# Optimization experiments

Hardware: AMD Instinct MI355X
Metric: run time of the kernel (lower is better)

Reference implementation:

```python
import jax, jax.numpy as jnp
import numpy as np

B, N, C = 4, 2048, 2048
H = 16
D = C // H  # head dim = 128


def setup_inputs() -> dict:
    key = jax.random.key(0)
    ks = jax.random.split(key, 5)
    s = 1.0 / np.sqrt(C)
    x = jax.random.normal(ks[0], (B, N, C), dtype=jnp.float32)
    w_qkv = jax.random.normal(ks[1], (C, 3 * C), dtype=jnp.float32) * s
    b_qkv = jax.random.normal(ks[2], (3 * C,), dtype=jnp.float32) * 0.01
    w_proj = jax.random.normal(ks[3], (C, C), dtype=jnp.float32) * s
    b_proj = jax.random.normal(ks[4], (C,), dtype=jnp.float32) * 0.01
    return {"x": x, "w_qkv": w_qkv, "b_qkv": b_qkv, "w_proj": w_proj, "b_proj": b_proj}


def reference(x, w_qkv, b_qkv, w_proj, b_proj):
    scale = D ** (-0.5)
    qkv = x @ w_qkv + b_qkv                              # [B,N,3C]
    qkv = qkv.reshape(B, N, 3, H, D).transpose(2, 0, 3, 1, 4)  # [3,B,H,N,D]
    q, k, v = qkv[0], qkv[1], qkv[2]
    attn = jnp.einsum('bhnd,bhmd->bhnm', q, k) * scale   # [B,H,N,N]
    attn = jax.nn.softmax(attn, axis=-1)
    out = jnp.einsum('bhnm,bhmd->bhnd', attn, v)         # [B,H,N,D]
    out = out.transpose(0, 2, 1, 3).reshape(B, N, C)
    return out @ w_proj + b_proj
```

## Files before the change

### kernel.cpp

```cpp
#include <hip/hip_runtime.h>

typedef short bf16x8 __attribute__((ext_vector_type(8)));
typedef float f32x4 __attribute__((ext_vector_type(4)));
typedef float f32x16 __attribute__((ext_vector_type(16)));
typedef unsigned int u32x4 __attribute__((ext_vector_type(4)));
typedef unsigned short u16;
typedef unsigned int u32;

__device__ __forceinline__ u16 f2bf(float f) {
  unsigned u = __builtin_bit_cast(unsigned, f);
  u += 0x7fffu + ((u >> 16) & 1u);
  return (u16)(u >> 16);
}

__device__ __forceinline__ void async16(const void* g, void* l) {
  __builtin_amdgcn_global_load_lds(
      (const __attribute__((address_space(1))) void*)g,
      (__attribute__((address_space(3))) void*)l, 16, 0, 0);
}

__global__ __launch_bounds__(256) void k_cvt(const float* __restrict__ src,
                                             u16* __restrict__ dst, int n4) {
  int i = blockIdx.x * blockDim.x + threadIdx.x;
  int stride = gridDim.x * blockDim.x;
  for (; i < n4; i += stride) {
    float4 f = ((const float4*)src)[i];
    ushort4 o;
    o.x = f2bf(f.x); o.y = f2bf(f.y); o.z = f2bf(f.z); o.w = f2bf(f.w);
    ((ushort4*)dst)[i] = o;
  }
}

__global__ __launch_bounds__(256) void k_tcvt(const float* __restrict__ src,
                                              u16* __restrict__ dst,
                                              int R, int C) {
  __shared__ float tile[64][65];
  int c0 = blockIdx.x * 64, r0 = blockIdx.y * 64;
  int tx = threadIdx.x & 63, ty = threadIdx.x >> 6;
#pragma unroll
  for (int i = 0; i < 64; i += 4)
    tile[ty + i][tx] = src[(size_t)(r0 + ty + i) * C + c0 + tx];
  __syncthreads();
#pragma unroll
  for (int i = 0; i < 64; i += 4)
    dst[(size_t)(c0 + ty + i) * R + r0 + tx] = f2bf(tile[tx][ty + i]);
}


__device__ __forceinline__ void stage_tile(u16* lds, const u16* gsrc, int tid) {
  const int r0 = tid >> 3, sl = tid & 7;
#pragma unroll
  for (int h = 0; h < 2; h++)
#pragma unroll
    for (int cc = 0; cc < 2; cc++) {
      int row = r0 + cc * 64;
      async16(gsrc + (size_t)(h * 128 + row) * 2048 + ((sl ^ (row & 7)) << 3),
              (char*)lds + ((size_t)(h * 1024 + row * 8 + sl) << 4));
    }
}

template <int QM>
__device__ __forceinline__ void rd_a(bf16x8 (&dst)[4][2], const u16* base,
                                     int lo, int g) {
#pragma unroll
  for (int m2 = 0; m2 < 4; m2++)
#pragma unroll
    for (int ks = 0; ks < 2; ks++) {
      int row = QM * 64 + m2 * 16 + lo;
      dst[m2][ks] = *(const bf16x8*)((const char*)base + row * 128 +
                                     (((ks * 4 + g) ^ (row & 7)) << 4));
    }
}

template <int QN>
__device__ __forceinline__ void rd_b(bf16x8 (&dst)[2][2], const u16* base,
                                     int brow_base, int lo, int g) {
#pragma unroll
  for (int n2 = 0; n2 < 2; n2++)
#pragma unroll
    for (int ks = 0; ks < 2; ks++) {
      int row = brow_base + QN * 32 + n2 * 16 + lo;
      dst[n2][ks] = *(const bf16x8*)((const char*)base + row * 128 +
                                     (((ks * 4 + g) ^ (row & 7)) << 4));
    }
}

template <int QM, int QN>
__device__ __forceinline__ void do_mm(f32x4 (&acc)[8][4], bf16x8 (&fa)[4][2],
                                      bf16x8 (&fb)[2][2]) {
  __builtin_amdgcn_s_setprio(1);
#pragma unroll
  for (int m2 = 0; m2 < 4; m2++)
#pragma unroll
    for (int n2 = 0; n2 < 2; n2++)
#pragma unroll
      for (int ks = 0; ks < 2; ks++)
        acc[QM * 4 + m2][QN * 2 + n2] = __builtin_amdgcn_mfma_f32_16x16x32_bf16(
            fa[m2][ks], fb[n2][ks], acc[QM * 4 + m2][QN * 2 + n2], 0, 0, 0);
  __builtin_amdgcn_s_setprio(0);
}

template <int EPI, int NT>
__global__ __launch_bounds__(512, 2) void k_gemm(
    const u16* __restrict__ A, const u16* __restrict__ Bt,
    const float* __restrict__ bias,
    u16* __restrict__ qb, u16* __restrict__ kb, u16* __restrict__ vtb,
    float* __restrict__ fout) {
  __shared__ u16 aL[2][2][128 * 64];
  __shared__ u16 bL[2][2][128 * 64];
  const int tid = threadIdx.x;
  const int lane = tid & 63, w = tid >> 6;
  const int lo = lane & 15, g = lane >> 4;
  const int wm = w >> 2, wn = w & 3;
  const int brow_base = (wn & 1) * 64;
  const int nwg = NT * 32;
  const int swz = (blockIdx.x & 7) * (nwg >> 3) + (blockIdx.x >> 3);
  const int by = swz / NT, bx = swz % NT;
  const int rm0 = by * 256, cn0 = bx * 256;
  const u16* Ab = A + (size_t)rm0 * 2048;
  const u16* Bb = Bt + (size_t)cn0 * 2048;

  f32x4 acc[8][4];
#pragma unroll
  for (int i = 0; i < 8; i++)
#pragma unroll
    for (int j = 0; j < 4; j++) {
      acc[i][j][0] = 0.f; acc[i][j][1] = 0.f;
      acc[i][j][2] = 0.f; acc[i][j][3] = 0.f;
    }

  stage_tile(&aL[0][0][0], Ab, tid);
  stage_tile(&bL[0][0][0], Bb, tid);

  for (int it = 0; it < 16; ++it) {
#pragma unroll
    for (int tt = 0; tt < 2; ++tt) {
      const int tn = 2 * it + tt + 1;
      const u16* aS = &aL[tt][wm][0];
      const u16* bS = &bL[tt][wn >> 1][0];
      bf16x8 fa[4][2], fb0[2][2], fb1[2][2];
      if (tn < 32) {
        stage_tile(&aL[tt ^ 1][0][0], Ab + tn * 64, tid);
        stage_tile(&bL[tt ^ 1][0][0], Bb + tn * 64, tid);
        asm volatile("s_waitcnt vmcnt(8)" ::: "memory");
      } else {
        asm volatile("s_waitcnt vmcnt(0)" ::: "memory");
      }
      __builtin_amdgcn_s_barrier();
      rd_a<0>(fa, aS, lo, g);
      rd_b<0>(fb0, bS, brow_base, lo, g);
      asm volatile("s_waitcnt lgkmcnt(0)" ::: "memory");
      do_mm<0, 0>(acc, fa, fb0);
      rd_b<1>(fb1, bS, brow_base, lo, g);
      asm volatile("s_waitcnt lgkmcnt(0)" ::: "memory");
      do_mm<0, 1>(acc, fa, fb1);
      rd_a<1>(fa, aS, lo, g);
      asm volatile("s_waitcnt lgkmcnt(0)" ::: "memory");
      do_mm<1, 1>(acc, fa, fb1);
      do_mm<1, 0>(acc, fa, fb0);
      __builtin_amdgcn_s_barrier();
    }
  }

#pragma unroll
  for (int qi = 0; qi < 8; qi++) {
    const int rowb = rm0 + wm * 128 + (qi >> 2) * 64 + (qi & 3) * 16 + g * 4;
#pragma unroll
    for (int nj = 0; nj < 4; nj++) {
      const int col = cn0 + wn * 64 + (nj >> 1) * 32 + (nj & 1) * 16 + lo;
      const float bcol = bias[col];
      const float v0 = acc[qi][nj][0] + bcol, v1 = acc[qi][nj][1] + bcol;
      const float v2 = acc[qi][nj][2] + bcol, v3 = acc[qi][nj][3] + bcol;
      if constexpr (EPI == 0) {
        const int which = col >> 11;
        const int hc = col & 2047, d = hc & 127;
        const int bh = ((rowb >> 11) << 4) | (hc >> 7);
        if (which == 2) {
          ushort4 us;
          us.x = f2bf(v0); us.y = f2bf(v1); us.z = f2bf(v2); us.w = f2bf(v3);
          *(ushort4*)(vtb + (size_t)bh * 262144 + (size_t)d * 2048 +
                      (rowb & 2047)) = us;
        } else {
          u16* dst = (which == 0) ? qb : kb;
          const float sc = (which == 0) ? 0.12751743f : 1.0f;
          size_t base = (size_t)bh * 262144 + (size_t)(rowb & 2047) * 128 + d;
          dst[base] = f2bf(v0 * sc);
          dst[base + 128] = f2bf(v1 * sc);
          dst[base + 256] = f2bf(v2 * sc);
          dst[base + 384] = f2bf(v3 * sc);
        }
      } else {
        fout[(size_t)(rowb + 0) * 2048 + col] = v0;
        fout[(size_t)(rowb + 1) * 2048 + col] = v1;
        fout[(size_t)(rowb + 2) * 2048 + col] = v2;
        fout[(size_t)(rowb + 3) * 2048 + col] = v3;
      }
    }
  }
}

__global__ __launch_bounds__(512) void k_attn(
    const u16* __restrict__ qg, const u16* __restrict__ kg,
    const u16* __restrict__ vtg, u16* __restrict__ og) {
  __shared__ u16 kt[2][64 * 128];
  __shared__ u16 vt[2][128 * 64];
  const int bh = blockIdx.x;
  const int b = bh >> 4, h = bh & 15;
  const u16* Q = qg + (size_t)bh * 262144;
  const u16* Kp = kg + (size_t)bh * 262144;
  const u16* VT = vtg + (size_t)bh * 262144;
  const int tid = threadIdx.x;
  const int lane = tid & 63, w = tid >> 6;
  const int ql = lane & 31, hi = lane >> 5;
  const int q0 = blockIdx.y * 256 + w * 32;

  const int c0 = tid, c1 = tid + 512;
  const int kva = c0 >> 4, ksa = c0 & 15, kvb = c1 >> 4, ksb = c1 & 15;
  const size_t koff_a = (size_t)kva * 128 + (size_t)((ksa ^ (kva & 7)) * 8);
  const size_t koff_b = (size_t)kvb * 128 + (size_t)((ksb ^ (kvb & 7)) * 8);
  const int da = c0 >> 3, sva = c0 & 7, db = c1 >> 3, svb = c1 & 7;
  const size_t voff_a = (size_t)da * 2048 + (size_t)((sva ^ (da & 7)) * 8);
  const size_t voff_b = (size_t)db * 2048 + (size_t)((svb ^ (db & 7)) * 8);

  bf16x8 qf[8];
#pragma unroll
  for (int c = 0; c < 8; c++)
    qf[c] = *(const bf16x8*)(Q + (size_t)(q0 + ql) * 128 + c * 16 + hi * 8);

  f32x16 o[4];
#pragma unroll
  for (int nd = 0; nd < 4; nd++)
#pragma unroll
    for (int r = 0; r < 16; r++) o[nd][r] = 0.f;
  float m = -1e30f, l = 0.f;

  {
    async16(Kp + koff_a, &kt[0][c0 * 8]);
    async16(Kp + koff_b, &kt[0][c1 * 8]);
    async16(VT + voff_a, &vt[0][c0 * 8]);
    async16(VT + voff_b, &vt[0][c1 * 8]);
  }
  int cur = 0;
  for (int kv0 = 0; kv0 < 2048; kv0 += 64) {
    __syncthreads();
    if (kv0 + 64 < 2048) {
      const u16* kbp = Kp + (size_t)(kv0 + 64) * 128;
      const u16* vbp = VT + (kv0 + 64);
      int nx = cur ^ 1;
      async16(kbp + koff_a, &kt[nx][c0 * 8]);
      async16(kbp + koff_b, &kt[nx][c1 * 8]);
      async16(vbp + voff_a, &vt[nx][c0 * 8]);
      async16(vbp + voff_b, &vt[nx][c1 * 8]);
    }
    const char* ktb = (const char*)&kt[cur][0];
    const char* vtb = (const char*)&vt[cur][0];

    f32x16 sacc[2];
#pragma unroll
    for (int s2 = 0; s2 < 2; s2++)
#pragma unroll
      for (int r = 0; r < 16; r++) sacc[s2][r] = 0.f;
    __builtin_amdgcn_s_setprio(1);
#pragma unroll
    for (int c = 0; c < 8; c++)
#pragma unroll
      for (int s2 = 0; s2 < 2; s2++) {
        int kv = s2 * 32 + ql;
        int phys = kv * 256 + ((c * 32 + hi * 16) ^ ((kv & 7) << 4));
        bf16x8 kf = *(const bf16x8*)(ktb + phys);
        sacc[s2] = __builtin_amdgcn_mfma_f32_32x32x16_bf16(kf, qf[c], sacc[s2], 0, 0, 0);
      }
    __builtin_amdgcn_s_setprio(0);

    float tm = sacc[0][0];
#pragma unroll
    for (int r = 1; r < 16; r++) tm = fmaxf(tm, sacc[0][r]);
#pragma unroll
    for (int r = 0; r < 16; r++) tm = fmaxf(tm, sacc[1][r]);
    tm = fmaxf(tm, __shfl_xor(tm, 32));
    if (!__all(tm <= m)) {
      float mnew = fmaxf(m, tm);
      float corr = exp2f(m - mnew);
      l *= corr;
#pragma unroll
      for (int nd = 0; nd < 4; nd++)
#pragma unroll
        for (int r = 0; r < 16; r++) o[nd][r] *= corr;
      m = mnew;
    }
    float ps = 0.f;
#pragma unroll
    for (int s2 = 0; s2 < 2; s2++)
#pragma unroll
      for (int r = 0; r < 16; r++) {
        float p = exp2f(sacc[s2][r] - m);
        sacc[s2][r] = p;
        ps += p;
      }
    ps += __shfl_xor(ps, 32);
    l += ps;

    bf16x8 pf[4];
#pragma unroll
    for (int s2 = 0; s2 < 2; s2++) {
      u32 pk[8];
#pragma unroll
      for (int i = 0; i < 8; i++) {
        u32 t;
        asm("v_cvt_pk_bf16_f32 %0, %1, %2"
            : "=v"(t) : "v"(sacc[s2][2 * i]), "v"(sacc[s2][2 * i + 1]));
        pk[i] = t;
      }
#pragma unroll
      for (int ksl = 0; ksl < 2; ksl++) {
        u32 a0 = pk[4 * ksl + 0], b0 = pk[4 * ksl + 2];
        u32 a1 = pk[4 * ksl + 1], b1 = pk[4 * ksl + 3];
        asm("v_permlane32_swap_b32 %0, %1" : "+v"(a0), "+v"(b0));
        asm("v_permlane32_swap_b32 %0, %1" : "+v"(a1), "+v"(b1));
        u32x4 fr = {a0, a1, b0, b1};
        pf[s2 * 2 + ksl] = __builtin_bit_cast(bf16x8, fr);
      }
    }

    __builtin_amdgcn_s_setprio(1);
#pragma unroll
    for (int nd = 0; nd < 4; nd++)
#pragma unroll
      for (int ks = 0; ks < 4; ks++) {
        int d = nd * 32 + ql;
        int phys = d * 128 + ((ks * 32 + hi * 16) ^ ((d & 7) << 4));
        bf16x8 vf = *(const bf16x8*)(vtb + phys);
        o[nd] = __builtin_amdgcn_mfma_f32_32x32x16_bf16(vf, pf[ks], o[nd], 0, 0, 0);
      }
    __builtin_amdgcn_s_setprio(0);
    cur ^= 1;
  }

  float inv = 1.0f / l;
  size_t rowbase = ((size_t)(b * 2048 + q0 + ql)) * 2048 + h * 128 + hi * 4;
#pragma unroll
  for (int nd = 0; nd < 4; nd++)
#pragma unroll
    for (int j2 = 0; j2 < 4; j2++) {
      ushort4 us;
      us.x = f2bf(o[nd][4 * j2 + 0] * inv);
      us.y = f2bf(o[nd][4 * j2 + 1] * inv);
      us.z = f2bf(o[nd][4 * j2 + 2] * inv);
      us.w = f2bf(o[nd][4 * j2 + 3] * inv);
      *(ushort4*)(og + rowbase + nd * 32 + j2 * 8) = us;
    }
}

extern "C" void kernel_launch(void* const* d_in, const int* in_sizes, int n_in,
                              void* d_out, int out_size, void* d_ws, size_t ws_size,
                              hipStream_t stream) {
  const float* x      = (const float*)d_in[0];
  const float* w_qkv  = (const float*)d_in[1];
  const float* b_qkv  = (const float*)d_in[2];
  const float* w_proj = (const float*)d_in[3];
  const float* b_proj = (const float*)d_in[4];
  float* out = (float*)d_out;

  char* p = (char*)d_ws;
  u16* xb     = (u16*)p; p += (size_t)8192 * 2048 * 2;
  u16* wqkvT  = (u16*)p; p += (size_t)6144 * 2048 * 2;
  u16* wprojT = (u16*)p; p += (size_t)2048 * 2048 * 2;
  u16* qb     = (u16*)p; p += (size_t)64 * 2048 * 128 * 2;
  u16* kb     = (u16*)p; p += (size_t)64 * 2048 * 128 * 2;
  u16* vtb    = (u16*)p; p += (size_t)64 * 2048 * 128 * 2;

  k_cvt<<<2048, 256, 0, stream>>>(x, xb, (8192 * 2048) / 4);
  k_tcvt<<<dim3(6144 / 64, 2048 / 64), 256, 0, stream>>>(w_qkv, wqkvT, 2048, 6144);
  k_tcvt<<<dim3(2048 / 64, 2048 / 64), 256, 0, stream>>>(w_proj, wprojT, 2048, 2048);
  k_gemm<0, 24><<<768, 512, 0, stream>>>(xb, wqkvT, b_qkv, qb, kb, vtb, nullptr);
  k_attn<<<dim3(64, 8), 512, 0, stream>>>(qb, kb, vtb, xb);
  k_gemm<1, 8><<<256, 512, 0, stream>>>(xb, wprojT, b_proj, nullptr, nullptr, nullptr, out);
}
```

Baseline: 497.1 us.

## Process two 32-row query tiles per wave in attention, halving block threads

The attention kernel now launches 256 threads per block, and each wave handles 64 query rows as two 32-row tiles. Each K and V fragment read from LDS feeds two MFMAs, which halves LDS read traffic per FLOP and gives the scheduler more independent MFMA chains. Each thread now issues four async loads per buffer instead of two. The row-sum cross-lane reduction moves out of the loop into the epilogue. In exchange, register pressure roughly doubles (two sets of O accumulators and Q fragments), the launch bound is set to one block, and fewer waves are resident to hide latency.

New measurement: 562.5 us. +13.1%, slower.

```diff
diff --git a/kernel.cpp b/kernel.cpp
--- a/kernel.cpp
+++ b/kernel.cpp
@@ -199,7 +199,56 @@
   }
 }
 
-__global__ __launch_bounds__(512) void k_attn(
+__device__ __forceinline__ void softmax_pf(f32x16 (&sacc)[2], float& m,
+                                           float& l, f32x16 (&o)[4],
+                                           bf16x8 (&pf)[4]) {
+  float tm = sacc[0][0];
+#pragma unroll
+  for (int r = 1; r < 16; r++) tm = fmaxf(tm, sacc[0][r]);
+#pragma unroll
+  for (int r = 0; r < 16; r++) tm = fmaxf(tm, sacc[1][r]);
+  tm = fmaxf(tm, __shfl_xor(tm, 32));
+  if (!__all(tm <= m)) {
+    float mnew = fmaxf(m, tm);
+    float corr = exp2f(m - mnew);
+    l *= corr;
+#pragma unroll
+    for (int nd = 0; nd < 4; nd++)
+#pragma unroll
+      for (int r = 0; r < 16; r++) o[nd][r] *= corr;
+    m = mnew;
+  }
+#pragma unroll
+  for (int s2 = 0; s2 < 2; s2++)
+#pragma unroll
+    for (int r = 0; r < 16; r++) {
+      float p = exp2f(sacc[s2][r] - m);
+      sacc[s2][r] = p;
+      l += p;
+    }
+#pragma unroll
+  for (int s2 = 0; s2 < 2; s2++) {
+    u32 pk[8];
+#pragma unroll
+    for (int i = 0; i < 8; i++) {
+      u32 t;
+      asm("v_cvt_pk_bf16_f32 %0, %1, %2"
+          : "=v"(t) : "v"(sacc[s2][2 * i]), "v"(sacc[s2][2 * i + 1]));
+      pk[i] = t;
+    }
+#pragma unroll
+    for (int ksl = 0; ksl < 2; ksl++) {
+      u32 a0 = pk[4 * ksl + 0], b0 = pk[4 * ksl + 2];
+      u32 a1 = pk[4 * ksl + 1], b1 = pk[4 * ksl + 3];
+      asm("v_permlane32_swap_b32 %0, %1" : "+v"(a0), "+v"(b0));
+      asm("v_permlane32_swap_b32 %0, %1" : "+v"(a1), "+v"(b1));
+      u32x4 fr = {a0, a1, b0, b1};
+      pf[s2 * 2 + ksl] = __builtin_bit_cast(bf16x8, fr);
+    }
+  }
+}
+
+__global__ __launch_bounds__(256, 1) void k_attn(
     const u16* __restrict__ qg, const u16* __restrict__ kg,
     const u16* __restrict__ vtg, u16* __restrict__ og) {
   __shared__ u16 kt[2][64 * 128];
@@ -212,33 +261,40 @@
   const int tid = threadIdx.x;
   const int lane = tid & 63, w = tid >> 6;
   const int ql = lane & 31, hi = lane >> 5;
-  const int q0 = blockIdx.y * 256 + w * 32;
-
-  const int c0 = tid, c1 = tid + 512;
-  const int kva = c0 >> 4, ksa = c0 & 15, kvb = c1 >> 4, ksb = c1 & 15;
-  const size_t koff_a = (size_t)kva * 128 + (size_t)((ksa ^ (kva & 7)) * 8);
-  const size_t koff_b = (size_t)kvb * 128 + (size_t)((ksb ^ (kvb & 7)) * 8);
-  const int da = c0 >> 3, sva = c0 & 7, db = c1 >> 3, svb = c1 & 7;
-  const size_t voff_a = (size_t)da * 2048 + (size_t)((sva ^ (da & 7)) * 8);
-  const size_t voff_b = (size_t)db * 2048 + (size_t)((svb ^ (db & 7)) * 8);
-
-  bf16x8 qf[8];
-#pragma unroll
-  for (int c = 0; c < 8; c++)
-    qf[c] = *(const bf16x8*)(Q + (size_t)(q0 + ql) * 128 + c * 16 + hi * 8);
-
-  f32x16 o[4];
+  const int q0 = blockIdx.y * 256 + w * 64;
+
+  size_t koff[4], voff[4];
+  u16 *kdst[4], *vdst[4];
+#pragma unroll
+  for (int j = 0; j < 4; j++) {
+    int c = tid + j * 256;
+    int kv = c >> 4, s = c & 15;
+    koff[j] = (size_t)kv * 128 + (size_t)((s ^ (kv & 7)) * 8);
+    int d = c >> 3, sv = c & 7;
+    voff[j] = (size_t)d * 2048 + (size_t)((sv ^ (d & 7)) * 8);
+    kdst[j] = nullptr; vdst[j] = nullptr;
+    (void)kdst; (void)vdst;
+  }
+
+  bf16x8 qf0[8], qf1[8];
+#pragma unroll
+  for (int c = 0; c < 8; c++) {
+    qf0[c] = *(const bf16x8*)(Q + (size_t)(q0 + ql) * 128 + c * 16 + hi * 8);
+    qf1[c] = *(const bf16x8*)(Q + (size_t)(q0 + 32 + ql) * 128 + c * 16 + hi * 8);
+  }
+
+  f32x16 o0[4], o1[4];
 #pragma unroll
   for (int nd = 0; nd < 4; nd++)
 #pragma unroll
-    for (int r = 0; r < 16; r++) o[nd][r] = 0.f;
-  float m = -1e30f, l = 0.f;
-
-  {
-    async16(Kp + koff_a, &kt[0][c0 * 8]);
-    async16(Kp + koff_b, &kt[0][c1 * 8]);
-    async16(VT + voff_a, &vt[0][c0 * 8]);
-    async16(VT + voff_b, &vt[0][c1 * 8]);
+    for (int r = 0; r < 16; r++) { o0[nd][r] = 0.f; o1[nd][r] = 0.f; }
+  float m0 = -1e30f, l0 = 0.f, m1 = -1e30f, l1 = 0.f;
+
+#pragma unroll
+  for (int j = 0; j < 4; j++) {
+    int c = tid + j * 256;
+    async16(Kp + koff[j], &kt[0][c * 8]);
+    async16(VT + voff[j], &vt[0][c * 8]);
   }
   int cur = 0;
   for (int kv0 = 0; kv0 < 2048; kv0 += 64) {
@@ -247,19 +303,21 @@
       const u16* kbp = Kp + (size_t)(kv0 + 64) * 128;
       const u16* vbp = VT + (kv0 + 64);
       int nx = cur ^ 1;
-      async16(kbp + koff_a, &kt[nx][c0 * 8]);
-      async16(kbp + koff_b, &kt[nx][c1 * 8]);
-      async16(vbp + voff_a, &vt[nx][c0 * 8]);
-      async16(vbp + voff_b, &vt[nx][c1 * 8]);
+#pragma unroll
+      for (int j = 0; j < 4; j++) {
+        int c = tid + j * 256;
+        async16(kbp + koff[j], &kt[nx][c * 8]);
+        async16(vbp + voff[j], &vt[nx][c * 8]);
+      }
     }
     const char* ktb = (const char*)&kt[cur][0];
     const char* vtb = (const char*)&vt[cur][0];
 
-    f32x16 sacc[2];
+    f32x16 sa0[2], sa1[2];
 #pragma unroll
     for (int s2 = 0; s2 < 2; s2++)
 #pragma unroll
-      for (int r = 0; r < 16; r++) sacc[s2][r] = 0.f;
+      for (int r = 0; r < 16; r++) { sa0[s2][r] = 0.f; sa1[s2][r] = 0.f; }
     __builtin_amdgcn_s_setprio(1);
 #pragma unroll
     for (int c = 0; c < 8; c++)
@@ -268,59 +326,14 @@
         int kv = s2 * 32 + ql;
         int phys = kv * 256 + ((c * 32 + hi * 16) ^ ((kv & 7) << 4));
         bf16x8 kf = *(const bf16x8*)(ktb + phys);
-        sacc[s2] = __builtin_amdgcn_mfma_f32_32x32x16_bf16(kf, qf[c], sacc[s2], 0, 0, 0);
+        sa0[s2] = __builtin_amdgcn_mfma_f32_32x32x16_bf16(kf, qf0[c], sa0[s2], 0, 0, 0);
+        sa1[s2] = __builtin_amdgcn_mfma_f32_32x32x16_bf16(kf, qf1[c], sa1[s2], 0, 0, 0);
       }
     __builtin_amdgcn_s_setprio(0);
 
-    float tm = sacc[0][0];
-#pragma unroll
-    for (int r = 1; r < 16; r++) tm = fmaxf(tm, sacc[0][r]);
-#pragma unroll
-    for (int r = 0; r < 16; r++) tm = fmaxf(tm, sacc[1][r]);
-    tm = fmaxf(tm, __shfl_xor(tm, 32));
-    if (!__all(tm <= m)) {
-      float mnew = fmaxf(m, tm);
-      float corr = exp2f(m - mnew);
-      l *= corr;
-#pragma unroll
-      for (int nd = 0; nd < 4; nd++)
-#pragma unroll
-        for (int r = 0; r < 16; r++) o[nd][r] *= corr;
-      m = mnew;
-    }
-    float ps = 0.f;
-#pragma unroll
-    for (int s2 = 0; s2 < 2; s2++)
-#pragma unroll
-      for (int r = 0; r < 16; r++) {
-        float p = exp2f(sacc[s2][r] - m);
-        sacc[s2][r] = p;
-        ps += p;
-      }
-    ps += __shfl_xor(ps, 32);
-    l += ps;
-
-    bf16x8 pf[4];
-#pragma unroll
-    for (int s2 = 0; s2 < 2; s2++) {
-      u32 pk[8];
-#pragma unroll
-      for (int i = 0; i < 8; i++) {
-        u32 t;
-        asm("v_cvt_pk_bf16_f32 %0, %1, %2"
-            : "=v"(t) : "v"(sacc[s2][2 * i]), "v"(sacc[s2][2 * i + 1]));
-        pk[i] = t;
-      }
-#pragma unroll
-      for (int ksl = 0; ksl < 2; ksl++) {
-        u32 a0 = pk[4 * ksl + 0], b0 = pk[4 * ksl + 2];
-        u32 a1 = pk[4 * ksl + 1], b1 = pk[4 * ksl + 3];
-        asm("v_permlane32_swap_b32 %0, %1" : "+v"(a0), "+v"(b0));
-        asm("v_permlane32_swap_b32 %0, %1" : "+v"(a1), "+v"(b1));
-        u32x4 fr = {a0, a1, b0, b1};
-        pf[s2 * 2 + ksl] = __builtin_bit_cast(bf16x8, fr);
-      }
-    }
+    bf16x8 pf0[4], pf1[4];
+    softmax_pf(sa0, m0, l0, o0, pf0);
+    softmax_pf(sa1, m1, l1, o1, pf1);
 
     __builtin_amdgcn_s_setprio(1);
 #pragma unroll
@@ -330,25 +343,45 @@
         int d = nd * 32 + ql;
         int phys = d * 128 + ((ks * 32 + hi * 16) ^ ((d & 7) << 4));
         bf16x8 vf = *(const bf16x8*)(vtb + phys);
-        o[nd] = __builtin_amdgcn_mfma_f32_32x32x16_bf16(vf, pf[ks], o[nd], 0, 0, 0);
+        o0[nd] = __builtin_amdgcn_mfma_f32_32x32x16_bf16(vf, pf0[ks], o0[nd], 0, 0, 0);
+        o1[nd] = __builtin_amdgcn_mfma_f32_32x32x16_bf16(vf, pf1[ks], o1[nd], 0, 0, 0);
       }
     __builtin_amdgcn_s_setprio(0);
     cur ^= 1;
   }
 
-  float inv = 1.0f / l;
-  size_t rowbase = ((size_t)(b * 2048 + q0 + ql)) * 2048 + h * 128 + hi * 4;
-#pragma unroll
-  for (int nd = 0; nd < 4; nd++)
-#pragma unroll
-    for (int j2 = 0; j2 < 4; j2++) {
-      ushort4 us;
-      us.x = f2bf(o[nd][4 * j2 + 0] * inv);
-      us.y = f2bf(o[nd][4 * j2 + 1] * inv);
-      us.z = f2bf(o[nd][4 * j2 + 2] * inv);
-      us.w = f2bf(o[nd][4 * j2 + 3] * inv);
-      *(ushort4*)(og + rowbase + nd * 32 + j2 * 8) = us;
-    }
+  {
+    float lt = l0 + __shfl_xor(l0, 32);
+    float inv = 1.0f / lt;
+    size_t rowbase = ((size_t)(b * 2048 + q0 + ql)) * 2048 + h * 128 + hi * 4;
+#pragma unroll
+    for (int nd = 0; nd < 4; nd++)
+#pragma unroll
+      for (int j2 = 0; j2 < 4; j2++) {
+        ushort4 us;
+        us.x = f2bf(o0[nd][4 * j2 + 0] * inv);
+        us.y = f2bf(o0[nd][4 * j2 + 1] * inv);
+        us.z = f2bf(o0[nd][4 * j2 + 2] * inv);
+        us.w = f2bf(o0[nd][4 * j2 + 3] * inv);
+        *(ushort4*)(og + rowbase + nd * 32 + j2 * 8) = us;
+      }
+  }
+  {
+    float lt = l1 + __shfl_xor(l1, 32);
+    float inv = 1.0f / lt;
+    size_t rowbase = ((size_t)(b * 2048 + q0 + 32 + ql)) * 2048 + h * 128 + hi * 4;
+#pragma unroll
+    for (int nd = 0; nd < 4; nd++)
+#pragma unroll
+      for (int j2 = 0; j2 < 4; j2++) {
+        ushort4 us;
+        us.x = f2bf(o1[nd][4 * j2 + 0] * inv);
+        us.y = f2bf(o1[nd][4 * j2 + 1] * inv);
+        us.z = f2bf(o1[nd][4 * j2 + 2] * inv);
+        us.w = f2bf(o1[nd][4 * j2 + 3] * inv);
+        *(ushort4*)(og + rowbase + nd * 32 + j2 * 8) = us;
+      }
+  }
 }
 
 extern "C" void kernel_launch(void* const* d_in, const int* in_sizes, int n_in,
@@ -373,6 +406,6 @@
   k_tcvt<<<dim3(6144 / 64, 2048 / 64), 256, 0, stream>>>(w_qkv, wqkvT, 2048, 6144);
   k_tcvt<<<dim3(2048 / 64, 2048 / 64), 256, 0, stream>>>(w_proj, wprojT, 2048, 2048);
   k_gemm<0, 24><<<768, 512, 0, stream>>>(xb, wqkvT, b_qkv, qb, kb, vtb, nullptr);
-  k_attn<<<dim3(64, 8), 512, 0, stream>>>(qb, kb, vtb, xb);
+  k_attn<<<dim3(64, 8), 256, 0, stream>>>(qb, kb, vtb, xb);
   k_gemm<1, 8><<<256, 512, 0, stream>>>(xb, wprojT, b_proj, nullptr, nullptr, nullptr, out);
 }
```
